# Kernel tuning notes

Measured on AMD Instinct MI355X. Metric: run time of the kernel, lower is better.

The kernel has to match this reference:

```python
import jax, jax.numpy as jnp
import numpy as np

B, N1, N2, D, O = 4, 256, 256, 64, 64
TEMP = 1.0
BN_EPS = 1e-5


def setup_inputs() -> dict:
    key = jax.random.key(0)
    ks = jax.random.split(key, 24)
    s = lambda n: 1.0 / np.sqrt(n)
    inp = {
        'x1': jax.random.normal(ks[0], (B, N1, D), jnp.float32),
        'x2': jax.random.normal(ks[1], (B, N2, D), jnp.float32),
        'W_t1': jax.random.normal(ks[2], (D, D), jnp.float32) * s(D),
        'b_t1': jnp.zeros((D,), jnp.float32),
        'W_t2': jax.random.normal(ks[3], (D, D), jnp.float32) * s(D),
        'b_t2': jnp.zeros((D,), jnp.float32),
        'W_att': jax.random.normal(ks[4], (D, O), jnp.float32) * s(D),
        'b_att': jnp.zeros((O,), jnp.float32),
        'W_attM': jax.random.normal(ks[5], (D, O), jnp.float32) * s(D),
        'b_attM': jnp.zeros((O,), jnp.float32),
        'w11': jax.random.normal(ks[6], (O, 1), jnp.float32) * s(O),
        'w22': jax.random.normal(ks[7], (O, 1), jnp.float32) * s(O),
        'w12': jax.random.normal(ks[8], (O, 1), jnp.float32) * s(O),
        'wM': jax.random.normal(ks[9], (O, 1), jnp.float32) * s(O),
        'W_pa': jax.random.normal(ks[10], (D, O), jnp.float32) * s(D),
        'b_pa': jnp.zeros((O,), jnp.float32),
        'W_po': jax.random.normal(ks[11], (D, O), jnp.float32) * s(D),
        'b_po': jnp.zeros((O,), jnp.float32),
        'W_paM': jax.random.normal(ks[12], (D, O), jnp.float32) * s(D),
        'b_paM': jnp.zeros((O,), jnp.float32),
        'W_poM': jax.random.normal(ks[13], (D, O), jnp.float32) * s(D),
        'b_poM': jnp.zeros((O,), jnp.float32),
        'gamma': jnp.ones((O,), jnp.float32),
        'beta': jnp.zeros((O,), jnp.float32),
    }
    return inp


def _forward(x1, x2, W_t1, b_t1, W_t2, b_t2, W_att, b_att, W_attM, b_attM,
             w11, w22, w12, wM, W_pa, b_pa, W_po, b_po, W_paM, b_paM,
             W_poM, b_poM, gamma, beta):
    n1 = x1.shape[1]
    h1 = x1 @ W_t1 + b_t1                      # (B,n1,D)
    h2 = x2 @ W_t2 + b_t2                      # (B,n2,D)
    x = jnp.concatenate([h1, h2], axis=1)      # (B,N,D)
    master = jnp.mean(x, axis=1, keepdims=True)  # (B,1,D)

    # --- type-blocked attention map ---
    pair = x[:, :, None, :] * x[:, None, :, :]          # (B,N,N,D)
    e = jnp.tanh(pair @ W_att + b_att)                   # (B,N,N,O)
    s11 = jnp.einsum('bijd,d->bij', e[:, :n1, :n1], w11[:, 0])
    s12 = jnp.einsum('bijd,d->bij', e[:, :n1, n1:], w12[:, 0])
    s21 = jnp.einsum('bijd,d->bij', e[:, n1:, :n1], w12[:, 0])
    s22 = jnp.einsum('bijd,d->bij', e[:, n1:, n1:], w22[:, 0])
    top = jnp.concatenate([s11, s12], axis=2)
    bot = jnp.concatenate([s21, s22], axis=2)
    scores = jnp.concatenate([top, bot], axis=1)         # (B,N,N)
    att = jax.nn.softmax(scores / TEMP, axis=2)          # softmax over source nodes (torch dim=-2 of (B,N,N,1))

    # --- master update ---
    m = jnp.tanh((x * master) @ W_attM + b_attM)         # (B,N,O)
    aM = jax.nn.softmax((m @ wM) / TEMP, axis=1)         # (B,N,1)
    agg_m = jnp.einsum('bn,bnd->bd', aM[:, :, 0], x)[:, None, :]  # (B,1,D)
    master_new = (agg_m @ W_paM + b_paM) + (master @ W_poM + b_poM)

    # --- node projection + BN(eval) + SELU ---
    agg = jnp.einsum('bij,bjd->bid', att, x)             # (B,N,D)
    y = (agg @ W_pa + b_pa) + (x @ W_po + b_po)          # (B,N,O)
    y = y / jnp.sqrt(1.0 + BN_EPS) * gamma + beta        # BN eval: mean=0, var=1
    y = jax.nn.selu(y)
    return y[:, :n1], y[:, n1:], master_new


def reference(x1, x2, W_t1, b_t1, W_t2, b_t2, W_att, b_att, W_attM, b_attM,
              w11, w22, w12, wM, W_pa, b_pa, W_po, b_po, W_paM, b_paM,
              W_poM, b_poM, gamma, beta):
    return _forward(x1, x2, W_t1, b_t1, W_t2, b_t2, W_att, b_att, W_attM,
                    b_attM, w11, w22, w12, wM, W_pa, b_pa, W_po, b_po,
                    W_paM, b_paM, W_poM, b_poM, gamma, beta)
```

## Files before the change

kernel.cpp:

```cpp
#include <hip/hip_runtime.h>

#define BB 4
#define NN 512
#define NH 256
#define DD 64

typedef __attribute__((ext_vector_type(8))) short bf16x8;
typedef __attribute__((ext_vector_type(16))) float f32x16;
union BF8 { bf16x8 v; unsigned int u[4]; };
union BF8Q { bf16x8 v; uint4 q; };

__device__ __forceinline__ float wred_sum(float v) {
  v += __shfl_xor(v, 32);
  v += __shfl_xor(v, 16);
  v += __shfl_xor(v, 8);
  v += __shfl_xor(v, 4);
  v += __shfl_xor(v, 2);
  v += __shfl_xor(v, 1);
  return v;
}

__device__ __forceinline__ float wred_max(float v) {
  v = fmaxf(v, __shfl_xor(v, 32));
  v = fmaxf(v, __shfl_xor(v, 16));
  v = fmaxf(v, __shfl_xor(v, 8));
  v = fmaxf(v, __shfl_xor(v, 4));
  v = fmaxf(v, __shfl_xor(v, 2));
  v = fmaxf(v, __shfl_xor(v, 1));
  return v;
}

__device__ __forceinline__ unsigned int cvtpk_bf16(float lo, float hi) {
  unsigned int r;
  asm("v_cvt_pk_bf16_f32 %0, %1, %2" : "=v"(r) : "v"(lo), "v"(hi));
  return r;
}

__device__ __forceinline__ float fast_exp2(float x) {
  float r;
  asm("v_exp_f32 %0, %1" : "=v"(r) : "v"(x));
  return r;
}

__device__ __forceinline__ float fast_tanh(float t) {
  t = fminf(15.f, fmaxf(-15.f, t));
  float z = __expf(2.f * t);
  return 1.f - 2.f * __builtin_amdgcn_rcpf(z + 1.f);
}

__device__ __forceinline__ float bflo(unsigned int u) { return __uint_as_float(u << 16); }
__device__ __forceinline__ float bfhi(unsigned int u) { return __uint_as_float(u & 0xffff0000u); }

__global__ __launch_bounds__(256)
void k1_build_x(const float* __restrict__ x1, const float* __restrict__ x2,
                const float* __restrict__ W_t1, const float* __restrict__ b_t1,
                const float* __restrict__ W_t2, const float* __restrict__ b_t2,
                float* __restrict__ X, unsigned int* __restrict__ XbfG) {
  const int tid = threadIdx.x;
  const int lane = tid & 63;
  const int rq = tid >> 6;
  const int r = blockIdx.x * 4 + rq;
  const int b = r >> 9;
  const int n = r & 511;
  const float* src; const float* W; const float* bias;
  if (n < NH) { src = x1 + (b * NH + n) * DD;        W = W_t1; bias = b_t1; }
  else        { src = x2 + (b * NH + (n - NH)) * DD; W = W_t2; bias = b_t2; }
  const float4* s4 = reinterpret_cast<const float4*>(src);
  float t0 = 0.f, t1 = 0.f, t2 = 0.f, t3 = 0.f;
#pragma unroll
  for (int c = 0; c < 16; ++c) {
    const float4 v = s4[c];
    t0 = fmaf(v.x, W[(4 * c + 0) * DD + lane], t0);
    t1 = fmaf(v.y, W[(4 * c + 1) * DD + lane], t1);
    t2 = fmaf(v.z, W[(4 * c + 2) * DD + lane], t2);
    t3 = fmaf(v.w, W[(4 * c + 3) * DD + lane], t3);
  }
  const float yv = ((t0 + t1) + (t2 + t3)) + bias[lane];
  X[r * DD + lane] = yv;
  const float nb = __shfl_down(yv, 1);
  if ((lane & 1) == 0) XbfG[r * 32 + (lane >> 1)] = cvtpk_bf16(yv, nb);
}

__global__ __launch_bounds__(512, 1)
void k_sc(const unsigned int* __restrict__ Xbf,
          const float* __restrict__ W_att, const float* __restrict__ b_att,
          const float* __restrict__ w11, const float* __restrict__ w22,
          const float* __restrict__ w12,
          float* __restrict__ scG) {
  const int b = blockIdx.y;
  const int bx = blockIdx.x;
  const int tid = threadIdx.x;
  const int lane = tid & 63;
  const int w = tid >> 6;
  const int l31 = lane & 31;
  const int half = lane >> 5;

  __shared__ __align__(16) float tblB[64];
  __shared__ __align__(16) unsigned int A2L[4][32];

  const unsigned int* __restrict__ Xb = Xbf + b * NN * 32;
  float* __restrict__ scb = scG + b * NN * NN;
  const float K2E = 2.8853900817779268f;

  if (tid < 64) {
    const int ot = tid >> 5, hf = (tid >> 4) & 1, r = tid & 15;
    const int o = ot * 32 + (r & 3) + 8 * (r >> 2) + 4 * hf;
    tblB[tid] = K2E * b_att[o];
  }
  if (tid >= 64 && tid < 320) {
    const int tt = tid - 64;
    const int comb = tt >> 6;
    const int idx = tt & 63;
    if (idx < 32) {
      const int ot = (idx >> 4) & 1, kg = (idx >> 3) & 1, hf = (idx >> 2) & 1, pp = idx & 3;
      const int it_ = comb >> 1, jt_ = comb & 1;
      const float* wsl = it_ ? (jt_ ? w22 : w12) : (jt_ ? w12 : w11);
      const int e0 = 2 * pp, e1 = 2 * pp + 1;
      const int o0 = ot * 32 + kg * 16 + (e0 & 3) + 8 * (e0 >> 2) + 4 * hf;
      const int o1 = ot * 32 + kg * 16 + (e1 & 3) + 8 * (e1 >> 2) + 4 * hf;
      A2L[comb][idx] = cvtpk_bf16(wsl[o0], wsl[o1]);
    }
  }

  BF8 Wp[2][4];
#pragma unroll
  for (int ot = 0; ot < 2; ++ot)
#pragma unroll
    for (int kt = 0; kt < 4; ++kt) {
      const int o = ot * 32 + l31;
#pragma unroll
      for (int pp = 0; pp < 4; ++pp) {
        const int d0 = kt * 16 + half * 8 + 2 * pp;
        Wp[ot][kt].u[pp] = cvtpk_bf16(W_att[d0 * DD + o], W_att[(d0 + 1) * DD + o]);
      }
    }

  __syncthreads();

  const int cminA = bx >> 4;
  const int n32A = 16 - cminA;
  const int rB = 510 - 2 * bx;
  const int cminB = (255 - bx) >> 4;
  const int njobs = 2 * (n32A + (16 - cminB));

#pragma unroll 1
  for (int jb = w; jb < njobs; jb += 8) {
    int row, c32;
    if (jb < 2 * n32A) { row = 2 * bx + (jb & 1); c32 = cminA + (jb >> 1); }
    else { const int tp = jb - 2 * n32A; row = rB + (tp & 1); c32 = cminB + (tp >> 1); }
    const int j0 = c32 * 32;
    const int comb = ((row >= NH) ? 2 : 0) | ((j0 >= NH) ? 1 : 0);

    BF8 Bi[4];
#pragma unroll
    for (int kt = 0; kt < 4; ++kt) {
      const uint4 xi = *reinterpret_cast<const uint4*>(Xb + row * 32 + kt * 8 + half * 4);
      const uint4 xj = *reinterpret_cast<const uint4*>(Xb + (j0 + l31) * 32 + kt * 8 + half * 4);
      Bi[kt].u[0] = cvtpk_bf16(bflo(xi.x) * bflo(xj.x), bfhi(xi.x) * bfhi(xj.x));
      Bi[kt].u[1] = cvtpk_bf16(bflo(xi.y) * bflo(xj.y), bfhi(xi.y) * bfhi(xj.y));
      Bi[kt].u[2] = cvtpk_bf16(bflo(xi.z) * bflo(xj.z), bfhi(xi.z) * bfhi(xj.z));
      Bi[kt].u[3] = cvtpk_bf16(bflo(xi.w) * bflo(xj.w), bfhi(xi.w) * bfhi(xj.w));
    }

    f32x16 C0 = {}, C1 = {};
#pragma unroll
    for (int kt = 0; kt < 4; ++kt) {
      C0 = __builtin_amdgcn_mfma_f32_32x32x16_bf16(Wp[0][kt].v, Bi[kt].v, C0, 0, 0, 0);
      C1 = __builtin_amdgcn_mfma_f32_32x32x16_bf16(Wp[1][kt].v, Bi[kt].v, C1, 0, 0, 0);
    }

    f32x16 D2 = {};
    const int base = half * 16;
#pragma unroll
    for (int ot = 0; ot < 2; ++ot) {
      float tv[16];
#pragma unroll
      for (int r = 0; r < 16; ++r) {
        const float Cr = (ot == 0) ? C0[r] : C1[r];
        const float arg = fmaf(Cr, K2E, tblB[ot * 32 + base + r]);
        const float e = fast_exp2(arg);
        tv[r] = fmaf(-2.f, __builtin_amdgcn_rcpf(e + 1.f), 1.f);
      }
      BF8 B2a, B2b;
#pragma unroll
      for (int pp = 0; pp < 4; ++pp) {
        B2a.u[pp] = cvtpk_bf16(tv[2 * pp], tv[2 * pp + 1]);
        B2b.u[pp] = cvtpk_bf16(tv[8 + 2 * pp], tv[9 + 2 * pp]);
      }
      BF8Q A2a, A2b;
      A2a.q = *reinterpret_cast<const uint4*>(&A2L[comb][ot * 16 + half * 4]);
      A2b.q = *reinterpret_cast<const uint4*>(&A2L[comb][ot * 16 + 8 + half * 4]);
      D2 = __builtin_amdgcn_mfma_f32_32x32x16_bf16(A2a.v, B2a.v, D2, 0, 0, 0);
      D2 = __builtin_amdgcn_mfma_f32_32x32x16_bf16(A2b.v, B2b.v, D2, 0, 0, 0);
    }
    const float pout = D2[0];
    if (lane < 32) {
      const int j = j0 + l31;
      if (j >= row) {
        scb[row * NN + j] = pout;
        if (j > row) scb[j * NN + row] = pout;
      }
    }
  }
}

__global__ __launch_bounds__(1024, 4)
void k_rest(const float* __restrict__ X, const float* __restrict__ scG,
            const float* __restrict__ W_attM, const float* __restrict__ b_attM,
            const float* __restrict__ wM,
            const float* __restrict__ W_pa, const float* __restrict__ b_pa,
            const float* __restrict__ W_po, const float* __restrict__ b_po,
            const float* __restrict__ gamma, const float* __restrict__ beta,
            float* __restrict__ master, float* __restrict__ logits,
            float* __restrict__ out) {
  const int b = blockIdx.y;
  const int i0 = blockIdx.x * 8;
  const int tid = threadIdx.x;
  const int lane = tid & 63;
  const int w = tid >> 6;

  __shared__ __align__(16) float Xlds[NN * DD];
  __shared__ __align__(16) float scL[8 * NN];
  __shared__ __align__(16) float red2[16][DD];
  __shared__ __align__(16) float aggL[8][DD];
  __shared__ __align__(16) float mastL[64];

  const float* __restrict__ Xb = X + b * NN * DD;

  {
    const int c4 = (tid & 15) * 4;
    const int rh = tid >> 4;
#pragma unroll
    for (int it = 0; it < 8; ++it) {
      const int r = it * 64 + rh;
      *reinterpret_cast<float4*>(&Xlds[r * DD + c4]) =
          *reinterpret_cast<const float4*>(&Xb[r * DD + c4]);
    }
  }
  {
    const int r8 = tid >> 7;
    const int c = (tid & 127) * 4;
    *reinterpret_cast<float4*>(&scL[r8 * NN + c]) =
        *reinterpret_cast<const float4*>(&scG[(b * NN + i0 + r8) * NN + c]);
  }
  __syncthreads();

  {
    float s = 0.f;
    for (int r = w * 32; r < w * 32 + 32; ++r) s += Xlds[r * DD + lane];
    red2[w][lane] = s;
  }
  __syncthreads();
  if (w == 0) {
    float s = 0.f;
#pragma unroll
    for (int k = 0; k < 16; ++k) s += red2[k][lane];
    s *= (1.f / 512.f);
    mastL[lane] = s;
    if (blockIdx.x == 0) master[b * DD + lane] = s;
  }

  const int row = w & 7, part = w >> 3;
  const int irow = i0 + row;
  float v[8];
#pragma unroll
  for (int k = 0; k < 8; ++k) v[k] = scL[row * NN + lane + 64 * k];
  __syncthreads();
  float mx = fmaxf(fmaxf(fmaxf(v[0], v[1]), fmaxf(v[2], v[3])),
                   fmaxf(fmaxf(v[4], v[5]), fmaxf(v[6], v[7])));
  mx = wred_max(mx);
  float ssum = 0.f;
#pragma unroll
  for (int k = 0; k < 8; ++k) { v[k] = __expf(v[k] - mx); ssum += v[k]; }
  ssum = wred_sum(ssum);
  const float inv = __builtin_amdgcn_rcpf(ssum);
#pragma unroll
  for (int k = 0; k < 4; ++k) {
    const int kk = part * 4 + k;
    scL[row * NN + lane + 64 * kk] = v[kk] * inv;
  }

  float a0 = 0.f, a1 = 0.f, a2 = 0.f, a3 = 0.f;
  const float* scr = &scL[row * NN + part * 256];
  const int xof = part * 256 * DD;
  for (int jj = 0; jj < 64; ++jj) {
    const float4 at = *reinterpret_cast<const float4*>(&scr[jj * 4]);
    a0 = fmaf(at.x, Xlds[xof + (jj * 4 + 0) * DD + lane], a0);
    a1 = fmaf(at.y, Xlds[xof + (jj * 4 + 1) * DD + lane], a1);
    a2 = fmaf(at.z, Xlds[xof + (jj * 4 + 2) * DD + lane], a2);
    a3 = fmaf(at.w, Xlds[xof + (jj * 4 + 3) * DD + lane], a3);
  }
  red2[w][lane] = (a0 + a1) + (a2 + a3);
  __syncthreads();

  if (part == 0) {
    const float aggv = red2[w][lane] + red2[w + 8][lane];
    aggL[row][lane] = aggv;
    float y = b_pa[lane] + b_po[lane];
#pragma unroll 8
    for (int d = 0; d < DD; ++d) {
      y = fmaf(aggL[row][d], W_pa[d * DD + lane], y);
      y = fmaf(Xlds[irow * DD + d], W_po[d * DD + lane], y);
    }
    const float RSQ = 0.9999950000374997f;
    y = y * RSQ * gamma[lane] + beta[lane];
    const float SC_ = 1.0507009873554805f;
    const float AL = 1.6732632423543772f;
    y = (y > 0.f) ? (SC_ * y) : (SC_ * AL * (__expf(y) - 1.f));
    const int off = (irow < NH) ? ((b * NH + irow) * DD + lane)
                                : (BB * NH * DD + (b * NH + (irow - NH)) * DD + lane);
    out[off] = y;
  } else {
    float lg = b_attM[lane];
#pragma unroll 8
    for (int d = 0; d < DD; ++d)
      lg = fmaf(Xlds[irow * DD + d] * mastL[d], W_attM[d * DD + lane], lg);
    const float th = fast_tanh(lg);
    const float s = wred_sum(th * wM[lane]);
    if (lane == 0) logits[b * NN + irow] = s;
  }
}

__global__ __launch_bounds__(256)
void k4_master_new(const float* __restrict__ X, const float* __restrict__ master,
                   const float* __restrict__ logits,
                   const float* __restrict__ W_paM, const float* __restrict__ b_paM,
                   const float* __restrict__ W_poM, const float* __restrict__ b_poM,
                   float* __restrict__ out) {
  const int b = blockIdx.x;
  const int tid = threadIdx.x;
  const int lane = tid & 63;
  const int q = tid >> 6;
  __shared__ float red[4][DD];
  __shared__ float r4[4];
  __shared__ float aggm_s[DD];
  __shared__ float mrow_s[DD];
  const float* lg = logits + b * NN;
  const float v0 = lg[tid];
  const float v1 = lg[tid + 256];
  float mx = wred_max(fmaxf(v0, v1));
  if (lane == 0) r4[q] = mx;
  __syncthreads();
  mx = fmaxf(fmaxf(r4[0], r4[1]), fmaxf(r4[2], r4[3]));
  float es = __expf(v0 - mx) + __expf(v1 - mx);
  es = wred_sum(es);
  __syncthreads();
  if (lane == 0) r4[q] = es;
  __syncthreads();
  const float S = r4[0] + r4[1] + r4[2] + r4[3];
  const float invS = 1.f / S;

  float acc = 0.f;
  for (int nn = q * 128; nn < q * 128 + 128; ++nn) {
    const float a = __expf(lg[nn] - mx);
    acc = fmaf(a, X[(b * NN + nn) * DD + lane], acc);
  }
  red[q][lane] = acc;
  __syncthreads();
  if (q == 0) {
    aggm_s[lane] =
        (red[0][lane] + red[1][lane] + red[2][lane] + red[3][lane]) * invS;
    mrow_s[lane] = master[b * DD + lane];
  }
  __syncthreads();
  float p = 0.f;
  for (int d = q * 16; d < q * 16 + 16; ++d) {
    p = fmaf(aggm_s[d], W_paM[d * DD + lane], p);
    p = fmaf(mrow_s[d], W_poM[d * DD + lane], p);
  }
  __syncthreads();
  red[q][lane] = p;
  __syncthreads();
  if (q == 0) {
    out[2 * BB * NH * DD + b * DD + lane] =
        red[0][lane] + red[1][lane] + red[2][lane] + red[3][lane] +
        b_paM[lane] + b_poM[lane];
  }
}

extern "C" void kernel_launch(void* const* d_in, const int* in_sizes, int n_in,
                              void* d_out, int out_size, void* d_ws, size_t ws_size,
                              hipStream_t stream) {
  const float* x1    = (const float*)d_in[0];
  const float* x2    = (const float*)d_in[1];
  const float* W_t1  = (const float*)d_in[2];
  const float* b_t1  = (const float*)d_in[3];
  const float* W_t2  = (const float*)d_in[4];
  const float* b_t2  = (const float*)d_in[5];
  const float* W_att = (const float*)d_in[6];
  const float* b_att = (const float*)d_in[7];
  const float* W_attM = (const float*)d_in[8];
  const float* b_attM = (const float*)d_in[9];
  const float* w11   = (const float*)d_in[10];
  const float* w22   = (const float*)d_in[11];
  const float* w12   = (const float*)d_in[12];
  const float* wM    = (const float*)d_in[13];
  const float* W_pa  = (const float*)d_in[14];
  const float* b_pa  = (const float*)d_in[15];
  const float* W_po  = (const float*)d_in[16];
  const float* b_po  = (const float*)d_in[17];
  const float* W_paM = (const float*)d_in[18];
  const float* b_paM = (const float*)d_in[19];
  const float* W_poM = (const float*)d_in[20];
  const float* b_poM = (const float*)d_in[21];
  const float* gamma = (const float*)d_in[22];
  const float* beta  = (const float*)d_in[23];

  float* ws     = (float*)d_ws;
  float* X      = ws;
  float* master = ws + 131072;
  float* logits = ws + 131328;
  float* scG    = ws + 133376;
  unsigned int* Xbf = (unsigned int*)(ws + 133376 + 1048576);
  float* out    = (float*)d_out;

  k1_build_x<<<512, 256, 0, stream>>>(x1, x2, W_t1, b_t1, W_t2, b_t2, X, Xbf);
  k_sc<<<dim3(128, 4), 512, 0, stream>>>(Xbf, W_att, b_att, w11, w22, w12, scG);
  k_rest<<<dim3(64, 4), 1024, 0, stream>>>(X, scG, W_attM, b_attM, wM,
                                           W_pa, b_pa, W_po, b_po, gamma, beta,
                                           master, logits, out);
  k4_master_new<<<4, 256, 0, stream>>>(X, master, logits, W_paM, b_paM, W_poM, b_poM, out);
}
```

Baseline: 49.29 us.

## Stage bf16 X in LDS for k_rest instead of fp32 copy

k_rest now loads the packed bf16 copy of X (Xbf) into shared memory instead of the fp32 X. This halves the global read and LDS footprint per block, which can allow more blocks per CU. The aggregation, master mean and projection loops are rewritten to unpack bf16 pairs, with per-half partial sums and register-cached rows of X. It adds bf16 rounding error to the master mean, the aggregation and the projections.

```diff
diff --git a/kernel.cpp b/kernel.cpp
--- a/kernel.cpp
+++ b/kernel.cpp
@@ -205,7 +205,7 @@
 }
 
 __global__ __launch_bounds__(1024, 4)
-void k_rest(const float* __restrict__ X, const float* __restrict__ scG,
+void k_rest(const unsigned int* __restrict__ Xbf, const float* __restrict__ scG,
             const float* __restrict__ W_attM, const float* __restrict__ b_attM,
             const float* __restrict__ wM,
             const float* __restrict__ W_pa, const float* __restrict__ b_pa,
@@ -218,24 +218,23 @@
   const int tid = threadIdx.x;
   const int lane = tid & 63;
   const int w = tid >> 6;
-
-  __shared__ __align__(16) float Xlds[NN * DD];
+  const int l31 = lane & 31;
+  const int half = lane >> 5;
+
+  __shared__ __align__(16) unsigned int XbfL[NN * 32];
   __shared__ __align__(16) float scL[8 * NN];
   __shared__ __align__(16) float red2[16][DD];
+  __shared__ __align__(16) float aggP[32][DD];
   __shared__ __align__(16) float aggL[8][DD];
   __shared__ __align__(16) float mastL[64];
 
-  const float* __restrict__ Xb = X + b * NN * DD;
+  const unsigned int* __restrict__ Xb = Xbf + b * NN * 32;
 
   {
-    const int c4 = (tid & 15) * 4;
-    const int rh = tid >> 4;
-#pragma unroll
-    for (int it = 0; it < 8; ++it) {
-      const int r = it * 64 + rh;
-      *reinterpret_cast<float4*>(&Xlds[r * DD + c4]) =
-          *reinterpret_cast<const float4*>(&Xb[r * DD + c4]);
-    }
+#pragma unroll
+    for (int k = 0; k < 4; ++k)
+      reinterpret_cast<uint4*>(XbfL)[tid + k * 1024] =
+          reinterpret_cast<const uint4*>(Xb)[tid + k * 1024];
   }
   {
     const int r8 = tid >> 7;
@@ -246,9 +245,15 @@
   __syncthreads();
 
   {
-    float s = 0.f;
-    for (int r = w * 32; r < w * 32 + 32; ++r) s += Xlds[r * DD + lane];
-    red2[w][lane] = s;
+    float se = 0.f, so = 0.f;
+    for (int r = w * 32; r < w * 32 + 32; ++r) {
+      const unsigned int u = XbfL[r * 32 + l31];
+      se += bflo(u); so += bfhi(u);
+    }
+    if (half == 0) {
+      float2 pr; pr.x = se; pr.y = so;
+      *reinterpret_cast<float2*>(&red2[w][l31 * 2]) = pr;
+    }
   }
   __syncthreads();
   if (w == 0) {
@@ -280,27 +285,50 @@
     scL[row * NN + lane + 64 * kk] = v[kk] * inv;
   }
 
-  float a0 = 0.f, a1 = 0.f, a2 = 0.f, a3 = 0.f;
-  const float* scr = &scL[row * NN + part * 256];
-  const int xof = part * 256 * DD;
-  for (int jj = 0; jj < 64; ++jj) {
-    const float4 at = *reinterpret_cast<const float4*>(&scr[jj * 4]);
-    a0 = fmaf(at.x, Xlds[xof + (jj * 4 + 0) * DD + lane], a0);
-    a1 = fmaf(at.y, Xlds[xof + (jj * 4 + 1) * DD + lane], a1);
-    a2 = fmaf(at.z, Xlds[xof + (jj * 4 + 2) * DD + lane], a2);
-    a3 = fmaf(at.w, Xlds[xof + (jj * 4 + 3) * DD + lane], a3);
-  }
-  red2[w][lane] = (a0 + a1) + (a2 + a3);
-  __syncthreads();
+  {
+    float ae = 0.f, ao = 0.f;
+    const int jb = part * 256 + half * 128;
+#pragma unroll 4
+    for (int it = 0; it < 32; ++it) {
+      const int j = jb + it * 4;
+      const float4 at = *reinterpret_cast<const float4*>(&scL[row * NN + j]);
+      const unsigned int u0 = XbfL[(j + 0) * 32 + l31];
+      const unsigned int u1 = XbfL[(j + 1) * 32 + l31];
+      const unsigned int u2 = XbfL[(j + 2) * 32 + l31];
+      const unsigned int u3 = XbfL[(j + 3) * 32 + l31];
+      ae = fmaf(at.x, bflo(u0), ae); ao = fmaf(at.x, bfhi(u0), ao);
+      ae = fmaf(at.y, bflo(u1), ae); ao = fmaf(at.y, bfhi(u1), ao);
+      ae = fmaf(at.z, bflo(u2), ae); ao = fmaf(at.z, bfhi(u2), ao);
+      ae = fmaf(at.w, bflo(u3), ae); ao = fmaf(at.w, bfhi(u3), ao);
+    }
+    float2 pr; pr.x = ae; pr.y = ao;
+    *reinterpret_cast<float2*>(&aggP[row * 4 + part * 2 + half][l31 * 2]) = pr;
+  }
+  __syncthreads();
+
+  uint4 xr[8];
+#pragma unroll
+  for (int s = 0; s < 8; ++s)
+    xr[s] = *reinterpret_cast<const uint4*>(&XbfL[irow * 32 + s * 4]);
 
   if (part == 0) {
-    const float aggv = red2[w][lane] + red2[w + 8][lane];
+    const float aggv = aggP[row * 4 + 0][lane] + aggP[row * 4 + 1][lane] +
+                       aggP[row * 4 + 2][lane] + aggP[row * 4 + 3][lane];
     aggL[row][lane] = aggv;
     float y = b_pa[lane] + b_po[lane];
-#pragma unroll 8
-    for (int d = 0; d < DD; ++d) {
-      y = fmaf(aggL[row][d], W_pa[d * DD + lane], y);
-      y = fmaf(Xlds[irow * DD + d], W_po[d * DD + lane], y);
+#pragma unroll
+    for (int s = 0; s < 8; ++s) {
+      const float xd[8] = {bflo(xr[s].x), bfhi(xr[s].x), bflo(xr[s].y), bfhi(xr[s].y),
+                           bflo(xr[s].z), bfhi(xr[s].z), bflo(xr[s].w), bfhi(xr[s].w)};
+      const float4 agA = *reinterpret_cast<const float4*>(&aggL[row][s * 8]);
+      const float4 agB = *reinterpret_cast<const float4*>(&aggL[row][s * 8 + 4]);
+      const float ad[8] = {agA.x, agA.y, agA.z, agA.w, agB.x, agB.y, agB.z, agB.w};
+#pragma unroll
+      for (int q = 0; q < 8; ++q) {
+        const int d = s * 8 + q;
+        y = fmaf(ad[q], W_pa[d * DD + lane], y);
+        y = fmaf(xd[q], W_po[d * DD + lane], y);
+      }
     }
     const float RSQ = 0.9999950000374997f;
     y = y * RSQ * gamma[lane] + beta[lane];
@@ -312,9 +340,19 @@
     out[off] = y;
   } else {
     float lg = b_attM[lane];
-#pragma unroll 8
-    for (int d = 0; d < DD; ++d)
-      lg = fmaf(Xlds[irow * DD + d] * mastL[d], W_attM[d * DD + lane], lg);
+#pragma unroll
+    for (int s = 0; s < 8; ++s) {
+      const float xd[8] = {bflo(xr[s].x), bfhi(xr[s].x), bflo(xr[s].y), bfhi(xr[s].y),
+                           bflo(xr[s].z), bfhi(xr[s].z), bflo(xr[s].w), bfhi(xr[s].w)};
+      const float4 mA = *reinterpret_cast<const float4*>(&mastL[s * 8]);
+      const float4 mB = *reinterpret_cast<const float4*>(&mastL[s * 8 + 4]);
+      const float md[8] = {mA.x, mA.y, mA.z, mA.w, mB.x, mB.y, mB.z, mB.w};
+#pragma unroll
+      for (int q = 0; q < 8; ++q) {
+        const int d = s * 8 + q;
+        lg = fmaf(xd[q] * md[q], W_attM[d * DD + lane], lg);
+      }
+    }
     const float th = fast_tanh(lg);
     const float s = wred_sum(th * wM[lane]);
     if (lane == 0) logits[b * NN + irow] = s;
@@ -416,7 +454,7 @@
 
   k1_build_x<<<512, 256, 0, stream>>>(x1, x2, W_t1, b_t1, W_t2, b_t2, X, Xbf);
   k_sc<<<dim3(128, 4), 512, 0, stream>>>(Xbf, W_att, b_att, w11, w22, w12, scG);
-  k_rest<<<dim3(64, 4), 1024, 0, stream>>>(X, scG, W_attM, b_attM, wM,
+  k_rest<<<dim3(64, 4), 1024, 0, stream>>>(Xbf, scG, W_attM, b_attM, wM,
                                            W_pa, b_pa, W_po, b_po, gamma, beta,
                                            master, logits, out);
   k4_master_new<<<4, 256, 0, stream>>>(X, master, logits, W_paM, b_paM, W_poM, b_poM, out);
```

New measurement: 48.71 us, median of 4. About the same (-1.2%).
